# Optimization experiments

Hardware: AMD Instinct MI355X
Metric: run time of the kernel (lower is better)

## Reference

```python
import jax, jax.numpy as jnp
import numpy as np

D_MODEL = 1024
N_HEADS = 16
HEAD_DIM = D_MODEL // N_HEADS


def setup_inputs() -> dict:
    key = jax.random.key(0)
    k_x, k_qkv, k_out = jax.random.split(key, 3)
    B, T = 4, 2048
    x = jax.random.normal(k_x, (B, T, D_MODEL), dtype=jnp.float32)
    # nn.Linear weight is (out, in); we store transposed (in, out) for x @ W
    s = 1.0 / np.sqrt(D_MODEL)
    W_qkv = jax.random.uniform(k_qkv, (D_MODEL, 3 * D_MODEL), dtype=jnp.float32, minval=-s, maxval=s)
    W_out = jax.random.uniform(k_out, (D_MODEL, D_MODEL), dtype=jnp.float32, minval=-s, maxval=s)
    return {"x": x, "W_qkv": W_qkv, "W_out": W_out}


def reference(x, W_qkv, W_out):
    B, T, C = x.shape
    H, Dh = N_HEADS, HEAD_DIM
    qkv = x @ W_qkv                                   # (B,T,3C)
    q, k, v = jnp.split(qkv, 3, axis=-1)
    # (B,T,C) -> (B,H,T,Dh)
    def split_heads(t):
        return t.reshape(B, T, H, Dh).transpose(0, 2, 1, 3)
    q, k, v = split_heads(q), split_heads(k), split_heads(v)
    scale = 1.0 / np.sqrt(Dh).astype(np.float32)
    scores = jnp.einsum('bhqd,bhkd->bhqk', q, k) * scale  # (B,H,T,T)
    causal = jnp.triu(jnp.ones((T, T), dtype=bool), k=1)   # True above diag
    scores = jnp.where(causal, -jnp.inf, scores)
    attn = jax.nn.softmax(scores, axis=-1)
    out = jnp.einsum('bhqk,bhkd->bhqd', attn, v)       # (B,H,T,Dh)
    out = out.transpose(0, 2, 1, 3).reshape(B, T, C)
    return out @ W_out
```

## Files before the change

kernel.cpp:

```cpp
#include <hip/hip_runtime.h>
#include <stdint.h>

#define T_ 2048
#define BB_ 4

typedef __bf16 bf16x8 __attribute__((ext_vector_type(8)));
typedef float f32x4 __attribute__((ext_vector_type(4)));
typedef unsigned short u16x8 __attribute__((ext_vector_type(8)));
typedef unsigned int u32x2 __attribute__((ext_vector_type(2)));
typedef unsigned int u32x4 __attribute__((ext_vector_type(4)));

__device__ __forceinline__ unsigned short f2b(float f) {
    unsigned int u = __builtin_bit_cast(unsigned int, f);
    return (unsigned short)((u + 0x7fffu + ((u >> 16) & 1u)) >> 16);
}

__device__ __forceinline__ unsigned cvt_pk(float lo, float hi) {
    unsigned r;
    asm("v_cvt_pk_bf16_f32 %0, %1, %2" : "=v"(r) : "v"(lo), "v"(hi));
    return r;
}

__device__ __forceinline__ void gload16(const void* g, const void* lds) {
    __builtin_amdgcn_global_load_lds(
        (__attribute__((address_space(1))) void*)(uintptr_t)g,
        (__attribute__((address_space(3))) void*)(uintptr_t)(unsigned int)(uintptr_t)lds,
        16, 0, 0);
}

__device__ __forceinline__ bf16x8 ld_b8(const unsigned short* p) {
    return *(const bf16x8*)p;
}

#define MFMA16(a, b, c) __builtin_amdgcn_mfma_f32_16x16x32_bf16((a), (b), (c), 0, 0, 0)

__global__ __launch_bounds__(256) void k_cvt(const float* __restrict__ in,
                                             unsigned short* __restrict__ out, int n) {
    int i = (blockIdx.x * 256 + threadIdx.x) * 4;
    const int stride = gridDim.x * 256 * 4;
    for (; i < n; i += stride) {
        const float4 v = *(const float4*)(in + i);
        ushort4 o = make_ushort4(f2b(v.x), f2b(v.y), f2b(v.z), f2b(v.w));
        *(ushort4*)(out + i) = o;
    }
}

template <int K, int N>
__global__ __launch_bounds__(256) void k_cvt_T(const float* __restrict__ W,
                                               unsigned short* __restrict__ WT) {
    __shared__ unsigned short t_[64][72];
    const int nt = blockIdx.x % (N / 64), kt = blockIdx.x / (N / 64);
    const int tid = threadIdx.x;
    const int r = tid >> 2, c = (tid & 3) * 16;
    const float* src = W + (size_t)(kt * 64 + r) * N + nt * 64 + c;
#pragma unroll
    for (int j = 0; j < 16; j += 4) {
        float4 v = *(const float4*)(src + j);
        t_[r][c + j + 0] = f2b(v.x);
        t_[r][c + j + 1] = f2b(v.y);
        t_[r][c + j + 2] = f2b(v.z);
        t_[r][c + j + 3] = f2b(v.w);
    }
    __syncthreads();
    unsigned short* dst = WT + (size_t)(nt * 64 + r) * K + kt * 64 + c;
#pragma unroll
    for (int j = 0; j < 16; ++j) dst[j] = t_[c + j][r];
}

template <int MODE, int NCOLS>
__global__ __launch_bounds__(512, 2) void k_gemm256(
    const unsigned short* __restrict__ A, const unsigned short* __restrict__ Bt,
    void* __restrict__ Cv, unsigned short* __restrict__ vt2) {
    constexpr int K = 1024, NT = K / 64;
    __shared__ unsigned short Abuf[2][2][8192];
    __shared__ unsigned short Bbuf[2][8192];
    const int tid = threadIdx.x;
    const int lane = tid & 63, wid = tid >> 6;
    const int wr = wid >> 1, wc = wid & 1;
    const int l4 = lane >> 4, l15 = lane & 15;
    const int m0 = blockIdx.y * 256, n0 = blockIdx.x * 128;

    const int se0 = tid * 8, se1 = tid * 8 + 4096;
    const int r0_ = se0 >> 6, c0_ = (se0 & 63) ^ ((r0_ & 7) << 3);
    const int r1_ = se1 >> 6, c1_ = (se1 & 63) ^ ((r1_ & 7) << 3);

    f32x4 acc[4][4] = {};

    auto STAGE = [&](int t, int d) {
#pragma unroll
        for (int h = 0; h < 2; ++h) {
            const unsigned short* as = A + (size_t)(m0 + h * 128) * K + t * 64;
            gload16(as + (size_t)r0_ * K + c0_, &Abuf[d][h][se0]);
            gload16(as + (size_t)r1_ * K + c1_, &Abuf[d][h][se1]);
        }
        const unsigned short* bs = Bt + (size_t)n0 * K + t * 64;
        gload16(bs + (size_t)r0_ * K + c0_, &Bbuf[d][se0]);
        gload16(bs + (size_t)r1_ * K + c1_, &Bbuf[d][se1]);
    };

    auto swz = [](const unsigned short* base, int row, int col) {
        int byte = row * 128 + col * 2;
        byte ^= (row & 7) << 4;
        return (const unsigned short*)((const char*)base + byte);
    };

    STAGE(0, 0);
    STAGE(1, 1);
    for (int t = 0; t < NT; ++t) {
        if (t == NT - 1)
            asm volatile("s_waitcnt vmcnt(0)" ::: "memory");
        else
            asm volatile("s_waitcnt vmcnt(6)" ::: "memory");
        __builtin_amdgcn_sched_barrier(0);
        __builtin_amdgcn_s_barrier();
        __builtin_amdgcn_sched_barrier(0);
        const unsigned short* Ah = &Abuf[t & 1][wr >> 1][0];
        const unsigned short* Bh = &Bbuf[t & 1][0];
#pragma unroll
        for (int ks = 0; ks < 2; ++ks) {
            bf16x8 af[4], bfr[4];
#pragma unroll
            for (int m = 0; m < 4; ++m)
                af[m] = ld_b8(swz(Ah, (wr & 1) * 64 + m * 16 + l15, ks * 32 + l4 * 8));
#pragma unroll
            for (int n = 0; n < 4; ++n)
                bfr[n] = ld_b8(swz(Bh, wc * 64 + n * 16 + l15, ks * 32 + l4 * 8));
            __builtin_amdgcn_s_setprio(1);
#pragma unroll
            for (int m = 0; m < 4; ++m)
#pragma unroll
                for (int n = 0; n < 4; ++n)
                    acc[m][n] = MFMA16(af[m], bfr[n], acc[m][n]);
            __builtin_amdgcn_s_setprio(0);
            __builtin_amdgcn_sched_barrier(0);
        }
        __builtin_amdgcn_s_barrier();
        __builtin_amdgcn_sched_barrier(0);
        if (t + 2 < NT) STAGE(t + 2, t & 1);
    }

    const int crow0 = m0 + wr * 64 + l4 * 4;
    const int ccol0 = n0 + wc * 64 + l15;
    if (MODE == 0 && n0 >= 2048) {
#pragma unroll
        for (int m = 0; m < 4; ++m)
#pragma unroll
            for (int n = 0; n < 4; ++n) {
                const int row = crow0 + m * 16;
                const int c = ccol0 + n * 16 - 2048;
                const int b = row >> 11, tt = row & 2047;
                const int h = c >> 6, dh = c & 63;
                ushort4 o;
                o.x = f2b(acc[m][n][0]);
                o.y = f2b(acc[m][n][1]);
                o.z = f2b(acc[m][n][2]);
                o.w = f2b(acc[m][n][3]);
                *(ushort4*)(vt2 + (size_t)(b * 16 + h) * 131072 + (tt >> 2) * 256 +
                            dh * 4) = o;
            }
    } else {
#pragma unroll
        for (int m = 0; m < 4; ++m)
#pragma unroll
            for (int n = 0; n < 4; ++n)
#pragma unroll
                for (int r = 0; r < 4; ++r) {
                    const size_t idx =
                        (size_t)(crow0 + m * 16 + r) * NCOLS + ccol0 + n * 16;
                    if (MODE == 1)
                        ((float*)Cv)[idx] = acc[m][n][r];
                    else
                        ((unsigned short*)Cv)[idx] = f2b(acc[m][n][r]);
                }
    }
}

__global__ __launch_bounds__(256) void k_attn(const unsigned short* __restrict__ qkv,
                                              const unsigned short* __restrict__ vt2,
                                              unsigned short* __restrict__ ao) {
    __shared__ unsigned short Ks[2 * 4096];
    __shared__ unsigned short Vs[2 * 4096];
    const int bh = blockIdx.x & 63;
    const int p = blockIdx.x >> 6;
    const int b = bh >> 4, h = bh & 15;
    const int tid = threadIdx.x, lane = tid & 63, w = tid >> 6;
    const int l4 = lane >> 4, l15 = lane & 15;

    const int sr0 = w * 16 + (lane >> 3);
    const int scol = 8 * ((lane & 7) ^ (lane >> 3));
    const unsigned short* Kg = qkv + (size_t)(b * T_) * 3072 + 1024 + h * 64;

    const unsigned short* Vg = vt2 + (size_t)bh * 131072;
    const int s0v = (w * 2 + 0) * 2 + (lane >> 5);
    const int s1v = (w * 2 + 1) * 2 + (lane >> 5);
    const unsigned short* vsrc0 =
        Vg + (4 * (s0v & 3) + (s0v >> 2)) * 256 + (lane & 31) * 8;
    const unsigned short* vsrc1 =
        Vg + (4 * (s1v & 3) + (s1v >> 2)) * 256 + (lane & 31) * 8;

    const u32x4 onesw = {0x3f803f80u, 0x3f803f80u, 0x3f803f80u, 0x3f803f80u};
    const bf16x8 ones = __builtin_bit_cast(bf16x8, onesw);

    for (int half = 0; half < 2; ++half) {
        const int qt = half ? p : 31 - p;

        const unsigned short* qb =
            qkv + (size_t)(b * T_ + qt * 64 + w * 16 + l15) * 3072 + h * 64;
        bf16x8 qf0, qf1;
        {
            const bf16x8 r0 = ld_b8(qb + l4 * 8);
            const bf16x8 r1 = ld_b8(qb + 32 + l4 * 8);
#pragma unroll
            for (int j = 0; j < 8; ++j) {
                qf0[j] = (__bf16)((float)r0[j] * 0.18033688f);
                qf1[j] = (__bf16)((float)r1[j] * 0.18033688f);
            }
        }

        f32x4 o[4] = {};
        f32x4 o_l = {};

        auto STAGE = [&](int kt, int bi) {
            unsigned short* Kb = Ks + bi * 4096;
            unsigned short* Vb = Vs + bi * 4096;
            gload16(Kg + (size_t)(kt * 64 + sr0) * 3072 + scol, Kb + (w * 2) * 512);
            gload16(Kg + (size_t)(kt * 64 + sr0 + 8) * 3072 + scol, Kb + (w * 2 + 1) * 512);
            gload16(vsrc0 + kt * 4096, Vb + (w * 2) * 512);
            gload16(vsrc1 + kt * 4096, Vb + (w * 2 + 1) * 512);
        };

        auto COMPUTE = [&](int bi, bool masked) {
            const unsigned short* Kb = Ks + bi * 4096;
            const unsigned short* Vb = Vs + bi * 4096;
            float tv[4][4];
            __builtin_amdgcn_s_setprio(1);
#pragma unroll
            for (int i = 0; i < 4; ++i) {
                const int key = i * 16 + l15;
                const int sw = (key & 7) << 4;
                const bf16x8 kf0 = ld_b8(Kb + (key * 128 + ((l4 * 16) ^ sw)) / 2);
                const bf16x8 kf1 = ld_b8(Kb + (key * 128 + ((l4 * 16 + 64) ^ sw)) / 2);
                f32x4 sacc = {};
                sacc = MFMA16(kf0, qf0, sacc);
                sacc = MFMA16(kf1, qf1, sacc);
#pragma unroll
                for (int r = 0; r < 4; ++r) tv[i][r] = sacc[r];
            }
            __builtin_amdgcn_s_setprio(0);
            if (masked) {
#pragma unroll
                for (int i = 0; i < 4; ++i)
#pragma unroll
                    for (int r = 0; r < 4; ++r)
                        if (i * 16 + l4 * 4 + r > w * 16 + l15) tv[i][r] = -1e30f;
            }
            unsigned pw[8];
#pragma unroll
            for (int i = 0; i < 4; ++i) {
                float pv[4];
#pragma unroll
                for (int r = 0; r < 4; ++r) pv[r] = __builtin_amdgcn_exp2f(tv[i][r]);
                pw[i * 2 + 0] = cvt_pk(pv[0], pv[1]);
                pw[i * 2 + 1] = cvt_pk(pv[2], pv[3]);
            }
            __builtin_amdgcn_s_setprio(1);
#pragma unroll
            for (int st = 0; st < 2; ++st) {
                const u32x4 pk = {pw[st * 4 + 0], pw[st * 4 + 1], pw[st * 4 + 2],
                                  pw[st * 4 + 3]};
                const bf16x8 pf = __builtin_bit_cast(bf16x8, pk);
                o_l = MFMA16(pf, ones, o_l);
#pragma unroll
                for (int ni = 0; ni < 4; ++ni) {
                    const unsigned short* vb =
                        Vb + (l4 * 4 + st * 2) * 256 + (ni * 16 + l15) * 4;
                    const u32x2 va = *(const u32x2*)vb;
                    const u32x2 vc = *(const u32x2*)(vb + 256);
                    const u32x4 vv = {va.x, va.y, vc.x, vc.y};
                    const bf16x8 vf = __builtin_bit_cast(bf16x8, vv);
                    o[ni] = MFMA16(pf, vf, o[ni]);
                }
            }
            __builtin_amdgcn_s_setprio(0);
        };

        __syncthreads();
        STAGE(0, 0);
        __syncthreads();
        for (int kt = 0; kt < qt; ++kt) {
            STAGE(kt + 1, (kt + 1) & 1);
            COMPUTE(kt & 1, false);
            __syncthreads();
        }
        COMPUTE(qt & 1, true);

        unsigned short* aop = ao + (size_t)(b * T_ + qt * 64 + w * 16) * 1024 + h * 64;
#pragma unroll
        for (int r = 0; r < 4; ++r) {
            const float inv = 1.0f / o_l[r];
#pragma unroll
            for (int ni = 0; ni < 4; ++ni)
                aop[(size_t)(l4 * 4 + r) * 1024 + ni * 16 + l15] = f2b(o[ni][r] * inv);
        }
    }
}

extern "C" void kernel_launch(void* const* d_in, const int* in_sizes, int n_in,
                              void* d_out, int out_size, void* d_ws, size_t ws_size,
                              hipStream_t stream) {
    (void)in_sizes; (void)n_in; (void)out_size; (void)ws_size;
    const float* x = (const float*)d_in[0];
    const float* Wqkv = (const float*)d_in[1];
    const float* Wout = (const float*)d_in[2];
    char* ws = (char*)d_ws;
    unsigned short* xb = (unsigned short*)(ws + 0);
    unsigned short* wqkvT = (unsigned short*)(ws + 16777216);
    unsigned short* woutT = (unsigned short*)(ws + 23068672);
    unsigned short* qkvb = (unsigned short*)(ws + 25165824);
    unsigned short* vt2 = (unsigned short*)(ws + 75497472);
    unsigned short* ao = (unsigned short*)(ws + 92274688);

    k_cvt<<<2048, 256, 0, stream>>>(x, xb, 4 * T_ * 1024);
    k_cvt_T<1024, 3072><<<16 * 48, 256, 0, stream>>>(Wqkv, wqkvT);
    k_cvt_T<1024, 1024><<<16 * 16, 256, 0, stream>>>(Wout, woutT);
    k_gemm256<0, 3072><<<dim3(24, 32), 512, 0, stream>>>(xb, wqkvT, qkvb, vt2);
    k_attn<<<1024, 256, 0, stream>>>(qkvb, vt2, ao);
    k_gemm256<1, 1024><<<dim3(8, 32), 512, 0, stream>>>(ao, woutT, d_out, nullptr);
}
```

Baseline: 158.1 us.

## Triple-buffer GEMM LDS and split prefetch across MFMA phases

Moves the 256x128 GEMM from double to triple LDS buffering, which removes the trailing barrier in each K iteration. The next-next tile's global-to-LDS loads are split into two halves, issued before and between the two MFMA k-sub-steps. All LDS fragments are loaded up front before the MFMAs. The LDS footprint grows to about 144KB per block, which likely limits each CU to one block instead of the two requested by the launch bounds.

After: 153.5 us. -2.9%, faster.

```diff
diff --git a/kernel.cpp b/kernel.cpp
--- a/kernel.cpp
+++ b/kernel.cpp
@@ -72,8 +72,8 @@
     const unsigned short* __restrict__ A, const unsigned short* __restrict__ Bt,
     void* __restrict__ Cv, unsigned short* __restrict__ vt2) {
     constexpr int K = 1024, NT = K / 64;
-    __shared__ unsigned short Abuf[2][2][8192];
-    __shared__ unsigned short Bbuf[2][8192];
+    __shared__ unsigned short Abuf[3][2][8192];
+    __shared__ unsigned short Bbuf[3][8192];
     const int tid = threadIdx.x;
     const int lane = tid & 63, wid = tid >> 6;
     const int wr = wid >> 1, wc = wid & 1;
@@ -86,15 +86,18 @@
 
     f32x4 acc[4][4] = {};
 
-    auto STAGE = [&](int t, int d) {
-#pragma unroll
-        for (int h = 0; h < 2; ++h) {
-            const unsigned short* as = A + (size_t)(m0 + h * 128) * K + t * 64;
-            gload16(as + (size_t)r0_ * K + c0_, &Abuf[d][h][se0]);
-            gload16(as + (size_t)r1_ * K + c1_, &Abuf[d][h][se1]);
-        }
+    auto STAGE1 = [&](int t, int d) {
+        const unsigned short* as = A + (size_t)m0 * K + t * 64;
+        gload16(as + (size_t)r0_ * K + c0_, &Abuf[d][0][se0]);
+        gload16(as + (size_t)r1_ * K + c1_, &Abuf[d][0][se1]);
         const unsigned short* bs = Bt + (size_t)n0 * K + t * 64;
         gload16(bs + (size_t)r0_ * K + c0_, &Bbuf[d][se0]);
+    };
+    auto STAGE2 = [&](int t, int d) {
+        const unsigned short* as = A + (size_t)(m0 + 128) * K + t * 64;
+        gload16(as + (size_t)r0_ * K + c0_, &Abuf[d][1][se0]);
+        gload16(as + (size_t)r1_ * K + c1_, &Abuf[d][1][se1]);
+        const unsigned short* bs = Bt + (size_t)n0 * K + t * 64;
         gload16(bs + (size_t)r1_ * K + c1_, &Bbuf[d][se1]);
     };
 
@@ -104,8 +107,11 @@
         return (const unsigned short*)((const char*)base + byte);
     };
 
-    STAGE(0, 0);
-    STAGE(1, 1);
+    STAGE1(0, 0);
+    STAGE2(0, 0);
+    STAGE1(1, 1);
+    STAGE2(1, 1);
+    int d = 0;
     for (int t = 0; t < NT; ++t) {
         if (t == NT - 1)
             asm volatile("s_waitcnt vmcnt(0)" ::: "memory");
@@ -114,29 +120,40 @@
         __builtin_amdgcn_sched_barrier(0);
         __builtin_amdgcn_s_barrier();
         __builtin_amdgcn_sched_barrier(0);
-        const unsigned short* Ah = &Abuf[t & 1][wr >> 1][0];
-        const unsigned short* Bh = &Bbuf[t & 1][0];
+        const int dn = (d + 2 >= 3) ? d - 1 : d + 2;
+        if (t + 2 < NT) STAGE1(t + 2, dn);
+        __builtin_amdgcn_sched_barrier(0);
+        const unsigned short* Ah = &Abuf[d][wr >> 1][0];
+        const unsigned short* Bh = &Bbuf[d][0];
+        bf16x8 af[2][4], bfr[2][4];
 #pragma unroll
         for (int ks = 0; ks < 2; ++ks) {
-            bf16x8 af[4], bfr[4];
 #pragma unroll
             for (int m = 0; m < 4; ++m)
-                af[m] = ld_b8(swz(Ah, (wr & 1) * 64 + m * 16 + l15, ks * 32 + l4 * 8));
+                af[ks][m] =
+                    ld_b8(swz(Ah, (wr & 1) * 64 + m * 16 + l15, ks * 32 + l4 * 8));
 #pragma unroll
             for (int n = 0; n < 4; ++n)
-                bfr[n] = ld_b8(swz(Bh, wc * 64 + n * 16 + l15, ks * 32 + l4 * 8));
-            __builtin_amdgcn_s_setprio(1);
-#pragma unroll
-            for (int m = 0; m < 4; ++m)
-#pragma unroll
-                for (int n = 0; n < 4; ++n)
-                    acc[m][n] = MFMA16(af[m], bfr[n], acc[m][n]);
-            __builtin_amdgcn_s_setprio(0);
-            __builtin_amdgcn_sched_barrier(0);
+                bfr[ks][n] = ld_b8(swz(Bh, wc * 64 + n * 16 + l15, ks * 32 + l4 * 8));
         }
-        __builtin_amdgcn_s_barrier();
-        __builtin_amdgcn_sched_barrier(0);
-        if (t + 2 < NT) STAGE(t + 2, t & 1);
+        __builtin_amdgcn_s_setprio(1);
+#pragma unroll
+        for (int m = 0; m < 4; ++m)
+#pragma unroll
+            for (int n = 0; n < 4; ++n)
+                acc[m][n] = MFMA16(af[0][m], bfr[0][n], acc[m][n]);
+        __builtin_amdgcn_s_setprio(0);
+        __builtin_amdgcn_sched_barrier(0);
+        if (t + 2 < NT) STAGE2(t + 2, dn);
+        __builtin_amdgcn_sched_barrier(0);
+        __builtin_amdgcn_s_setprio(1);
+#pragma unroll
+        for (int m = 0; m < 4; ++m)
+#pragma unroll
+            for (int n = 0; n < 4; ++n)
+                acc[m][n] = MFMA16(af[1][m], bfr[1][n], acc[m][n]);
+        __builtin_amdgcn_s_setprio(0);
+        d = (d + 1 == 3) ? 0 : d + 1;
     }
 
     const int crow0 = m0 + wr * 64 + l4 * 4;
```
